# Performance work log

Hardware: AMD Instinct MI355X
Metric: run time of the kernel (lower is better)

Reference implementation:

```python
import jax, jax.numpy as jnp
import numpy as np

DIM = 1024
DEPTH = 6
HEADS = 16
DH = 64
INNER = HEADS * DH  # 1024
MLP = 4096
B, N = 2, 2048
SCALE = DH ** (-0.5)  # 0.125; module divides softmax output by this (x8)
EPS = 1e-5


def setup_inputs() -> dict:
    key = jax.random.key(0)
    ks = jax.random.split(key, 5)
    s = jnp.float32(0.02)
    return {
        "x": jax.random.normal(ks[0], (B, N, DIM), dtype=jnp.float32),
        "ln1_g": jnp.ones((DEPTH, DIM), jnp.float32),
        "ln1_b": jnp.zeros((DEPTH, DIM), jnp.float32),
        "w_qkv": jax.random.normal(ks[1], (DEPTH, DIM, 3 * INNER), jnp.float32) * s,
        "w_out": jax.random.normal(ks[2], (DEPTH, INNER, DIM), jnp.float32) * s,
        "b_out": jnp.zeros((DEPTH, DIM), jnp.float32),
        "ln2_g": jnp.ones((DEPTH, DIM), jnp.float32),
        "ln2_b": jnp.zeros((DEPTH, DIM), jnp.float32),
        "w1": jax.random.normal(ks[3], (DEPTH, DIM, MLP), jnp.float32) * s,
        "b1": jnp.zeros((DEPTH, MLP), jnp.float32),
        "w2": jax.random.normal(ks[4], (DEPTH, MLP, DIM), jnp.float32) * s,
        "b2": jnp.zeros((DEPTH, DIM), jnp.float32),
    }


def _layernorm(x, g, b):
    m = x.mean(-1, keepdims=True)
    v = ((x - m) ** 2).mean(-1, keepdims=True)
    return (x - m) * jax.lax.rsqrt(v + EPS) * g + b


def _attention(x, w_qkv, w_out, b_out):
    b, n, _ = x.shape
    qkv = x @ w_qkv  # [b, n, 3*inner]
    q, k, v = jnp.split(qkv, 3, axis=-1)

    def heads(t):
        return t.reshape(b, n, HEADS, DH).transpose(0, 2, 1, 3)  # [b,h,n,d]

    q, k, v = heads(q), heads(k), heads(v)
    # Faithful to source: softmax of UNSCALED logits, then divide by scale.
    score = jax.nn.softmax(jnp.einsum("bhqd,bhkd->bhqk", q, k), axis=-1) / SCALE
    o = jnp.einsum("bhqk,bhkd->bhqd", score, v)
    o = o.transpose(0, 2, 1, 3).reshape(b, n, INNER)
    return o @ w_out + b_out


def reference(x, ln1_g, ln1_b, w_qkv, w_out, b_out, ln2_g, ln2_b, w1, b1, w2, b2):
    def layer(h, p):
        g1, bb1, wq, wo, bo, g2, bb2, ww1, bw1, ww2, bw2 = p
        h = h + _attention(_layernorm(h, g1, bb1), wq, wo, bo)
        f = _layernorm(h, g2, bb2) @ ww1 + bw1
        f = jax.nn.gelu(f, approximate=False)  # nn.GELU default = exact erf
        h = h + f @ ww2 + bw2
        return h, None

    out, _ = jax.lax.scan(
        layer, x, (ln1_g, ln1_b, w_qkv, w_out, b_out, ln2_g, ln2_b, w1, b1, w2, b2)
    )
    return out
```

## Files before the change

kernel.cpp:

```cpp
#include <hip/hip_runtime.h>
#include <cstdint>

typedef __attribute__((ext_vector_type(4))) float f32x4;
typedef __attribute__((ext_vector_type(8))) short short8;
typedef __attribute__((ext_vector_type(4))) short short4v;
typedef _Float16 half8v __attribute__((ext_vector_type(8)));

__device__ __forceinline__ unsigned short f2h(float x) {
  _Float16 h = (_Float16)x;
  return __builtin_bit_cast(unsigned short, h);
}
__device__ __forceinline__ unsigned int pk2(float a, float b) {
  auto h = __builtin_amdgcn_cvt_pkrtz(a, b);
  return __builtin_bit_cast(unsigned int, h);
}

template <typename V>
__device__ __forceinline__ auto mfma_impl(V a, V b, f32x4 c, int)
    -> decltype(__builtin_amdgcn_mfma_f32_16x16x32_f16(a, b, c, 0, 0, 0)) {
  return __builtin_amdgcn_mfma_f32_16x16x32_f16(a, b, c, 0, 0, 0);
}
template <typename V>
__device__ __forceinline__ f32x4 mfma_impl(V a, V b, f32x4 c, long) {
  return __builtin_amdgcn_mfma_f32_16x16x32_f16(
      __builtin_bit_cast(half8v, a), __builtin_bit_cast(half8v, b), c, 0, 0, 0);
}
__device__ __forceinline__ f32x4 MFMA(short8 a, short8 b, f32x4 c) {
  return mfma_impl(a, b, c, 0);
}

__device__ __forceinline__ void load_lds16(const void* g, void* l) {
  __builtin_amdgcn_global_load_lds(
      (__attribute__((address_space(1))) void*)(uintptr_t)g,
      (__attribute__((address_space(3))) void*)l, 16, 0, 0);
}

__global__ __launch_bounds__(256) void ln_f16_kernel(
    const float* __restrict__ X, const float* __restrict__ gam,
    const float* __restrict__ bet, unsigned short* __restrict__ Y) {
  __shared__ float red[8];
  const int row = blockIdx.x, t = threadIdx.x;
  const float4 v = ((const float4*)(X + (size_t)row * 1024))[t];
  float s = v.x + v.y + v.z + v.w;
#pragma unroll
  for (int o = 32; o >= 1; o >>= 1) s += __shfl_xor(s, o, 64);
  if ((t & 63) == 0) red[t >> 6] = s;
  __syncthreads();
  const float mean = (red[0] + red[1] + red[2] + red[3]) * (1.0f / 1024.0f);
  const float dx = v.x - mean, dy = v.y - mean, dz = v.z - mean, dw = v.w - mean;
  float ss = dx * dx + dy * dy + dz * dz + dw * dw;
#pragma unroll
  for (int o = 32; o >= 1; o >>= 1) ss += __shfl_xor(ss, o, 64);
  if ((t & 63) == 0) red[4 + (t >> 6)] = ss;
  __syncthreads();
  const float var = (red[4] + red[5] + red[6] + red[7]) * (1.0f / 1024.0f);
  const float rstd = rsqrtf(var + 1e-5f);
  const float4 gg = ((const float4*)gam)[t];
  const float4 bb = ((const float4*)bet)[t];
  ushort4 o4;
  o4.x = f2h(dx * rstd * gg.x + bb.x);
  o4.y = f2h(dy * rstd * gg.y + bb.y);
  o4.z = f2h(dz * rstd * gg.z + bb.z);
  o4.w = f2h(dw * rstd * gg.w + bb.w);
  ((ushort4*)(Y + (size_t)row * 1024))[t] = o4;
}

__global__ __launch_bounds__(256) void transpose_f16_kernel(
    const float* __restrict__ W, unsigned short* __restrict__ WT, int K, int N) {
  __shared__ float t[32][33];
  const int n0 = blockIdx.x * 32, k0 = blockIdx.y * 32;
  const int tx = threadIdx.x, ty = threadIdx.y;
#pragma unroll
  for (int i = 0; i < 4; ++i)
    t[ty + 8 * i][tx] = W[(size_t)(k0 + ty + 8 * i) * N + n0 + tx];
  __syncthreads();
#pragma unroll
  for (int i = 0; i < 4; ++i)
    WT[(size_t)(n0 + ty + 8 * i) * K + k0 + tx] = f2h(t[tx][ty + 8 * i]);
}

__global__ __launch_bounds__(256) void vt_transpose_kernel(
    const unsigned short* __restrict__ qkvb, unsigned short* __restrict__ VT) {
  __shared__ unsigned short t[32][33];
  const int c0 = blockIdx.x * 32;
  const int r0 = blockIdx.y * 32;
  const int b = blockIdx.z;
  const int tx = threadIdx.x, ty = threadIdx.y;
  const size_t base = (size_t)b * 2048;
#pragma unroll
  for (int i = 0; i < 4; ++i)
    t[ty + 8 * i][tx] = qkvb[(base + r0 + ty + 8 * i) * 3072 + 2048 + c0 + tx];
  __syncthreads();
#pragma unroll
  for (int i = 0; i < 4; ++i)
    VT[((size_t)b * 1024 + c0 + ty + 8 * i) * 2048 + r0 + tx] = t[tx][ty + 8 * i];
}

template <int BM, int EPI>
__global__ __launch_bounds__(256, BM == 64 ? 3 : 2) void gemm_f16_kernel(
    const unsigned short* __restrict__ A, const unsigned short* __restrict__ BT,
    void* Cout, const float* __restrict__ bias, const float* __restrict__ res,
    int M, int N, int K) {
  constexpr int BN = 128, BK = 64;
  constexpr int MR = BM / 32;
  constexpr int ACH = BM * BK / 8;
  constexpr int BCH = BN * BK / 8;
  __shared__ alignas(16) unsigned short a_sh[2][BM * BK];
  __shared__ alignas(16) unsigned short b_sh[2][BN * BK];
  const int tid = threadIdx.x;
  const int w = tid >> 6, lane = tid & 63, g = lane >> 4, lm = lane & 15;
  const int m0 = blockIdx.y * BM, n0 = blockIdx.x * BN;
  const int wm = (w >> 1) * (BM / 2), wn = (w & 1) * 64;
  f32x4 acc[MR][4] = {};
  const int nsteps = K >> 6;

  auto stage = [&](int buf, int kk) {
#pragma unroll
    for (int c0 = 0; c0 < ACH; c0 += 256) {
      const int c = c0 + tid, row = c >> 3;
      const int sc = (c & 7) ^ (row & 7);
      const int cb = c0 + (tid & 192);
      load_lds16(A + (size_t)(m0 + row) * K + kk + sc * 8, &a_sh[buf][cb * 8]);
    }
#pragma unroll
    for (int c0 = 0; c0 < BCH; c0 += 256) {
      const int c = c0 + tid, row = c >> 3;
      const int sc = (c & 7) ^ (row & 7);
      const int cb = c0 + (tid & 192);
      load_lds16(BT + (size_t)(n0 + row) * K + kk + sc * 8, &b_sh[buf][cb * 8]);
    }
  };

  stage(0, 0);
  __syncthreads();
  int cur = 0;
  for (int step = 0; step < nsteps; ++step) {
    if (step + 1 < nsteps) stage(cur ^ 1, (step + 1) * BK);
#pragma unroll
    for (int kc = 0; kc < 2; ++kc) {
      short8 af[MR], bfr[4];
#pragma unroll
      for (int i = 0; i < MR; ++i) {
        const int r = wm + i * 16 + lm;
        af[i] = *(const short8*)&a_sh[cur][r * 64 + (((kc << 2) | g) ^ (r & 7)) * 8];
      }
#pragma unroll
      for (int j = 0; j < 4; ++j) {
        const int r = wn + j * 16 + lm;
        bfr[j] = *(const short8*)&b_sh[cur][r * 64 + (((kc << 2) | g) ^ (r & 7)) * 8];
      }
#pragma unroll
      for (int i = 0; i < MR; ++i)
#pragma unroll
        for (int j = 0; j < 4; ++j)
          acc[i][j] = MFMA(af[i], bfr[j], acc[i][j]);
    }
    if (step + 1 < nsteps) {
      __syncthreads();
      cur ^= 1;
    }
  }

#pragma unroll
  for (int i = 0; i < MR; ++i) {
    const int row = m0 + wm + i * 16 + g * 4;
#pragma unroll
    for (int j = 0; j < 4; ++j) {
      const int col = n0 + wn + j * 16 + lm;
#pragma unroll
      for (int r = 0; r < 4; ++r) {
        const float v = acc[i][j][r];
        const size_t idx = (size_t)(row + r) * N + col;
        if (EPI == 0) {
          ((unsigned short*)Cout)[idx] = f2h(v);
        } else if (EPI == 1) {
          const float xx = v + bias[col];
          ((unsigned short*)Cout)[idx] =
              f2h(0.5f * xx * (1.0f + erff(xx * 0.70710678118654752f)));
        } else {
          ((float*)Cout)[idx] = res[idx] + v + bias[col];
        }
      }
    }
  }
}

__global__ __launch_bounds__(256) void attn_kernel(
    const unsigned short* __restrict__ qkv, const unsigned short* __restrict__ vt,
    unsigned short* __restrict__ obuf) {
  constexpr int PK = 72;
  constexpr int PV = 68;
  __shared__ alignas(16) unsigned short Qs[64 * PK];
  __shared__ alignas(16) unsigned short Ks[64 * PK];
  __shared__ alignas(16) unsigned short VsT[64 * PV];
  const int tid = threadIdx.x;
  const int w = tid >> 6, lane = tid & 63, g = lane >> 4, lm = lane & 15;
  const int qbase = blockIdx.x * 64, h = blockIdx.y, b = blockIdx.z;
  const size_t rowbase = (size_t)b * 2048;
  const int r0 = tid >> 3, cc = tid & 7;
  const int vd = tid >> 2, vk = tid & 3;
  const int kdst = r0 * PK + cc * 8;

  const unsigned short* qptr = qkv + (rowbase + qbase + r0) * 3072 + h * 64 + cc * 8;
#pragma unroll
  for (int s = 0; s < 2; ++s)
    *(uint4*)&Qs[(s * 32 + r0) * PK + cc * 8] = *(const uint4*)(qptr + (size_t)s * 32 * 3072);

  const unsigned short* kptr = qkv + (rowbase + r0) * 3072 + 1024 + h * 64 + cc * 8;
  const unsigned short* vtp = vt + ((size_t)b * 1024 + h * 64 + vd) * 2048 + vk * 16;
  uint4 kreg[2], vreg[2];
  auto load_tile = [&](int n) {
#pragma unroll
    for (int s = 0; s < 2; ++s) {
      kreg[s] = *(const uint4*)(kptr + (size_t)n * 64 * 3072 + (size_t)s * 32 * 3072);
      vreg[s] = *(const uint4*)(vtp + n * 64 + s * 8);
    }
  };
  auto write_tile = [&]() {
#pragma unroll
    for (int s = 0; s < 2; ++s) {
      *(uint4*)&Ks[kdst + s * 32 * PK] = kreg[s];
      uint2 lo; lo.x = vreg[s].x; lo.y = vreg[s].y;
      uint2 hi; hi.x = vreg[s].z; hi.y = vreg[s].w;
      *(uint2*)&VsT[vd * PV + vk * 16 + s * 8] = lo;
      *(uint2*)&VsT[vd * PV + vk * 16 + s * 8 + 4] = hi;
    }
  };

  load_tile(0);
  __syncthreads();
  short8 qf[2];
#pragma unroll
  for (int s2 = 0; s2 < 2; ++s2)
    qf[s2] = *(const short8*)&Qs[(w * 16 + lm) * PK + s2 * 32 + g * 8];

  float mrun = -1e30f, lrun = 0.0f;
  f32x4 accO[4] = {};

  for (int n = 0; n < 32; ++n) {
    __syncthreads();
    write_tile();
    __syncthreads();
    if (n + 1 < 32) load_tile(n + 1);

    f32x4 sf[4] = {};
    __builtin_amdgcn_s_setprio(1);
#pragma unroll
    for (int s2 = 0; s2 < 2; ++s2)
#pragma unroll
      for (int i = 0; i < 4; ++i) {
        const short8 kf = *(const short8*)&Ks[(i * 16 + lm) * PK + s2 * 32 + g * 8];
        sf[i] = MFMA(kf, qf[s2], sf[i]);
      }
    __builtin_amdgcn_s_setprio(0);

    float tmax = -1e30f;
#pragma unroll
    for (int i = 0; i < 4; ++i)
#pragma unroll
      for (int r = 0; r < 4; ++r) tmax = fmaxf(tmax, sf[i][r]);
    tmax = fmaxf(tmax, __shfl_xor(tmax, 16, 64));
    tmax = fmaxf(tmax, __shfl_xor(tmax, 32, 64));
    const float mnew = fmaxf(mrun, tmax);
    const float scale = __expf(mrun - mnew);
    float p[4][4];
    float psum = 0.0f;
#pragma unroll
    for (int i = 0; i < 4; ++i)
#pragma unroll
      for (int r = 0; r < 4; ++r) {
        p[i][r] = __expf(sf[i][r] - mnew);
        psum += p[i][r];
      }
    psum += __shfl_xor(psum, 16, 64);
    psum += __shfl_xor(psum, 32, 64);
    lrun = lrun * scale + psum;
    mrun = mnew;
#pragma unroll
    for (int t = 0; t < 4; ++t) accO[t] = accO[t] * scale;

    uint4 pbu[2];
#pragma unroll
    for (int blk = 0; blk < 2; ++blk) {
      pbu[blk].x = pk2(p[2 * blk][0], p[2 * blk][1]);
      pbu[blk].y = pk2(p[2 * blk][2], p[2 * blk][3]);
      pbu[blk].z = pk2(p[2 * blk + 1][0], p[2 * blk + 1][1]);
      pbu[blk].w = pk2(p[2 * blk + 1][2], p[2 * blk + 1][3]);
    }

    __builtin_amdgcn_s_setprio(1);
#pragma unroll
    for (int blk = 0; blk < 2; ++blk) {
      const short8 pbv = __builtin_bit_cast(short8, pbu[blk]);
#pragma unroll
      for (int t = 0; t < 4; ++t) {
        const int base = (16 * t + lm) * PV + 32 * blk + 4 * g;
        const short4v vlo = *(const short4v*)&VsT[base];
        const short4v vhi = *(const short4v*)&VsT[base + 16];
        const short8 vf = {vlo[0], vlo[1], vlo[2], vlo[3],
                           vhi[0], vhi[1], vhi[2], vhi[3]};
        accO[t] = MFMA(vf, pbv, accO[t]);
      }
    }
    __builtin_amdgcn_s_setprio(0);
  }

  const float inv = 8.0f / lrun;
  const size_t orow = rowbase + qbase + w * 16 + lm;
#pragma unroll
  for (int t = 0; t < 4; ++t) {
    ushort4 o4;
    o4.x = f2h(accO[t][0] * inv);
    o4.y = f2h(accO[t][1] * inv);
    o4.z = f2h(accO[t][2] * inv);
    o4.w = f2h(accO[t][3] * inv);
    *(ushort4*)&obuf[orow * 1024 + h * 64 + t * 16 + g * 4] = o4;
  }
}

extern "C" void kernel_launch(void* const* d_in, const int* in_sizes, int n_in,
                              void* d_out, int out_size, void* d_ws, size_t ws_size,
                              hipStream_t stream) {
  const float* x     = (const float*)d_in[0];
  const float* ln1_g = (const float*)d_in[1];
  const float* ln1_b = (const float*)d_in[2];
  const float* w_qkv = (const float*)d_in[3];
  const float* w_out = (const float*)d_in[4];
  const float* b_out = (const float*)d_in[5];
  const float* ln2_g = (const float*)d_in[6];
  const float* ln2_b = (const float*)d_in[7];
  const float* w1    = (const float*)d_in[8];
  const float* b1    = (const float*)d_in[9];
  const float* w2    = (const float*)d_in[10];
  const float* b2    = (const float*)d_in[11];
  float* h = (float*)d_out;

  char* ws = (char*)d_ws;
  const size_t MB = 1u << 20;
  unsigned short* xn   = (unsigned short*)(ws);
  unsigned short* ob   = (unsigned short*)(ws + 8 * MB);
  unsigned short* qkvb = (unsigned short*)(ws + 16 * MB);
  unsigned short* mid  = (unsigned short*)(ws + 40 * MB);
  unsigned short* wt   = (unsigned short*)(ws + 72 * MB);

  hipError_t e0 = hipMemcpyAsync(h, x, (size_t)4096 * 1024 * sizeof(float),
                                 hipMemcpyDeviceToDevice, stream);
  (void)e0;

  const dim3 tb(32, 8);
  for (int L = 0; L < 6; ++L) {
    const float* Lg1 = ln1_g + L * 1024;
    const float* Lb1 = ln1_b + L * 1024;
    const float* Lwq = w_qkv + (size_t)L * 1024 * 3072;
    const float* Lwo = w_out + (size_t)L * 1024 * 1024;
    const float* Lbo = b_out + L * 1024;
    const float* Lg2 = ln2_g + L * 1024;
    const float* Lb2 = ln2_b + L * 1024;
    const float* Lw1 = w1 + (size_t)L * 1024 * 4096;
    const float* Lb1m = b1 + L * 4096;
    const float* Lw2 = w2 + (size_t)L * 4096 * 1024;
    const float* Lb2m = b2 + L * 1024;

    ln_f16_kernel<<<4096, 256, 0, stream>>>(h, Lg1, Lb1, xn);
    transpose_f16_kernel<<<dim3(96, 32), tb, 0, stream>>>(Lwq, wt, 1024, 3072);
    gemm_f16_kernel<128, 0><<<dim3(24, 32), 256, 0, stream>>>(
        xn, wt, qkvb, nullptr, nullptr, 4096, 3072, 1024);
    vt_transpose_kernel<<<dim3(32, 64, 2), tb, 0, stream>>>(qkvb, xn);
    attn_kernel<<<dim3(32, 16, 2), 256, 0, stream>>>(qkvb, xn, ob);
    transpose_f16_kernel<<<dim3(32, 32), tb, 0, stream>>>(Lwo, wt, 1024, 1024);
    gemm_f16_kernel<64, 2><<<dim3(8, 64), 256, 0, stream>>>(
        ob, wt, h, Lbo, h, 4096, 1024, 1024);

    ln_f16_kernel<<<4096, 256, 0, stream>>>(h, Lg2, Lb2, xn);
    transpose_f16_kernel<<<dim3(128, 32), tb, 0, stream>>>(Lw1, wt, 1024, 4096);
    gemm_f16_kernel<128, 1><<<dim3(32, 32), 256, 0, stream>>>(
        xn, wt, mid, Lb1m, nullptr, 4096, 4096, 1024);
    transpose_f16_kernel<<<dim3(32, 128), tb, 0, stream>>>(Lw2, wt, 4096, 1024);
    gemm_f16_kernel<64, 2><<<dim3(8, 64), 256, 0, stream>>>(
        mid, wt, h, Lb2m, h, 4096, 1024, 4096);
  }
  (void)in_sizes; (void)n_in; (void)out_size; (void)ws_size;
}
```

Baseline: 1.845 ms.

## Merge per-layer weight transposes into one launch and widen attention KV tile

The four per-layer weight transpose/convert launches are merged into a single kernel that dispatches on block index and writes into separate workspace regions. This removes three launches per layer. The attention kernel now processes 128 keys per iteration instead of 64, halving the loop trips and barriers. It drops the separate Q shared buffer by staging Q in the K buffer, and loads V with wider 16-byte vectors. The larger tile raises register pressure, and the kernel now carries a launch-bounds occupancy hint of 4.

```diff
diff --git a/kernel.cpp b/kernel.cpp
--- a/kernel.cpp
+++ b/kernel.cpp
@@ -65,18 +65,28 @@
   ((ushort4*)(Y + (size_t)row * 1024))[t] = o4;
 }
 
-__global__ __launch_bounds__(256) void transpose_f16_kernel(
-    const float* __restrict__ W, unsigned short* __restrict__ WT, int K, int N) {
+__global__ __launch_bounds__(256) void transpose_all_kernel(
+    const float* __restrict__ wq, const float* __restrict__ wo,
+    const float* __restrict__ w1, const float* __restrict__ w2,
+    unsigned short* __restrict__ wtq, unsigned short* __restrict__ wto,
+    unsigned short* __restrict__ wt1, unsigned short* __restrict__ wt2) {
   __shared__ float t[32][33];
-  const int n0 = blockIdx.x * 32, k0 = blockIdx.y * 32;
+  int i = blockIdx.x;
+  const float* W; unsigned short* WT; int K, N;
+  if (i < 3072)      { W = wq; WT = wtq; K = 1024; N = 3072; }
+  else if (i < 4096) { i -= 3072; W = wo; WT = wto; K = 1024; N = 1024; }
+  else if (i < 8192) { i -= 4096; W = w1; WT = wt1; K = 1024; N = 4096; }
+  else               { i -= 8192; W = w2; WT = wt2; K = 4096; N = 1024; }
+  const int nt = N >> 5;
+  const int n0 = (i % nt) * 32, k0 = (i / nt) * 32;
   const int tx = threadIdx.x, ty = threadIdx.y;
 #pragma unroll
-  for (int i = 0; i < 4; ++i)
-    t[ty + 8 * i][tx] = W[(size_t)(k0 + ty + 8 * i) * N + n0 + tx];
-  __syncthreads();
-#pragma unroll
-  for (int i = 0; i < 4; ++i)
-    WT[(size_t)(n0 + ty + 8 * i) * K + k0 + tx] = f2h(t[tx][ty + 8 * i]);
+  for (int j = 0; j < 4; ++j)
+    t[ty + 8 * j][tx] = W[(size_t)(k0 + ty + 8 * j) * N + n0 + tx];
+  __syncthreads();
+#pragma unroll
+  for (int j = 0; j < 4; ++j)
+    WT[(size_t)(n0 + ty + 8 * j) * K + k0 + tx] = f2h(t[tx][ty + 8 * j]);
 }
 
 __global__ __launch_bounds__(256) void vt_transpose_kernel(
@@ -185,46 +195,44 @@
   }
 }
 
-__global__ __launch_bounds__(256) void attn_kernel(
+__global__ __launch_bounds__(256, 4) void attn_kernel(
     const unsigned short* __restrict__ qkv, const unsigned short* __restrict__ vt,
     unsigned short* __restrict__ obuf) {
   constexpr int PK = 72;
-  constexpr int PV = 68;
-  __shared__ alignas(16) unsigned short Qs[64 * PK];
-  __shared__ alignas(16) unsigned short Ks[64 * PK];
-  __shared__ alignas(16) unsigned short VsT[64 * PV];
+  constexpr int PV2 = 136;
+  __shared__ alignas(16) unsigned short Ks[128 * PK];
+  __shared__ alignas(16) unsigned short VsT[64 * PV2];
   const int tid = threadIdx.x;
   const int w = tid >> 6, lane = tid & 63, g = lane >> 4, lm = lane & 15;
   const int qbase = blockIdx.x * 64, h = blockIdx.y, b = blockIdx.z;
   const size_t rowbase = (size_t)b * 2048;
   const int r0 = tid >> 3, cc = tid & 7;
-  const int vd = tid >> 2, vk = tid & 3;
+  const int vd = tid >> 4, ch = tid & 15;
   const int kdst = r0 * PK + cc * 8;
 
   const unsigned short* qptr = qkv + (rowbase + qbase + r0) * 3072 + h * 64 + cc * 8;
 #pragma unroll
   for (int s = 0; s < 2; ++s)
-    *(uint4*)&Qs[(s * 32 + r0) * PK + cc * 8] = *(const uint4*)(qptr + (size_t)s * 32 * 3072);
+    *(uint4*)&Ks[(s * 32 + r0) * PK + cc * 8] = *(const uint4*)(qptr + (size_t)s * 32 * 3072);
 
   const unsigned short* kptr = qkv + (rowbase + r0) * 3072 + 1024 + h * 64 + cc * 8;
-  const unsigned short* vtp = vt + ((size_t)b * 1024 + h * 64 + vd) * 2048 + vk * 16;
-  uint4 kreg[2], vreg[2];
+  const unsigned short* vtp = vt + ((size_t)b * 1024 + h * 64 + vd) * 2048 + ch * 8;
+  uint4 kreg[4], vreg[4];
   auto load_tile = [&](int n) {
 #pragma unroll
-    for (int s = 0; s < 2; ++s) {
-      kreg[s] = *(const uint4*)(kptr + (size_t)n * 64 * 3072 + (size_t)s * 32 * 3072);
-      vreg[s] = *(const uint4*)(vtp + n * 64 + s * 8);
-    }
+    for (int s = 0; s < 4; ++s)
+      kreg[s] = *(const uint4*)(kptr + ((size_t)n * 128 + s * 32) * 3072);
+#pragma unroll
+    for (int s = 0; s < 4; ++s)
+      vreg[s] = *(const uint4*)(vtp + (size_t)s * 16 * 2048 + n * 128);
   };
   auto write_tile = [&]() {
 #pragma unroll
-    for (int s = 0; s < 2; ++s) {
-      *(uint4*)&Ks[kdst + s * 32 * PK] = kreg[s];
-      uint2 lo; lo.x = vreg[s].x; lo.y = vreg[s].y;
-      uint2 hi; hi.x = vreg[s].z; hi.y = vreg[s].w;
-      *(uint2*)&VsT[vd * PV + vk * 16 + s * 8] = lo;
-      *(uint2*)&VsT[vd * PV + vk * 16 + s * 8 + 4] = hi;
-    }
+    for (int s = 0; s < 4; ++s)
+      *(uint4*)&Ks[(s * 32 + r0) * PK + cc * 8] = kreg[s];
+#pragma unroll
+    for (int s = 0; s < 4; ++s)
+      *(uint4*)&VsT[(s * 16 + vd) * PV2 + ch * 8] = vreg[s];
   };
 
   load_tile(0);
@@ -232,23 +240,23 @@
   short8 qf[2];
 #pragma unroll
   for (int s2 = 0; s2 < 2; ++s2)
-    qf[s2] = *(const short8*)&Qs[(w * 16 + lm) * PK + s2 * 32 + g * 8];
+    qf[s2] = *(const short8*)&Ks[(w * 16 + lm) * PK + s2 * 32 + g * 8];
 
   float mrun = -1e30f, lrun = 0.0f;
   f32x4 accO[4] = {};
 
-  for (int n = 0; n < 32; ++n) {
+  for (int n = 0; n < 16; ++n) {
     __syncthreads();
     write_tile();
     __syncthreads();
-    if (n + 1 < 32) load_tile(n + 1);
-
-    f32x4 sf[4] = {};
+    if (n + 1 < 16) load_tile(n + 1);
+
+    f32x4 sf[8] = {};
     __builtin_amdgcn_s_setprio(1);
 #pragma unroll
     for (int s2 = 0; s2 < 2; ++s2)
 #pragma unroll
-      for (int i = 0; i < 4; ++i) {
+      for (int i = 0; i < 8; ++i) {
         const short8 kf = *(const short8*)&Ks[(i * 16 + lm) * PK + s2 * 32 + g * 8];
         sf[i] = MFMA(kf, qf[s2], sf[i]);
       }
@@ -256,22 +264,33 @@
 
     float tmax = -1e30f;
 #pragma unroll
-    for (int i = 0; i < 4; ++i)
+    for (int i = 0; i < 8; ++i)
 #pragma unroll
       for (int r = 0; r < 4; ++r) tmax = fmaxf(tmax, sf[i][r]);
     tmax = fmaxf(tmax, __shfl_xor(tmax, 16, 64));
     tmax = fmaxf(tmax, __shfl_xor(tmax, 32, 64));
     const float mnew = fmaxf(mrun, tmax);
     const float scale = __expf(mrun - mnew);
-    float p[4][4];
     float psum = 0.0f;
-#pragma unroll
-    for (int i = 0; i < 4; ++i)
+    uint4 pbu[4];
+#pragma unroll
+    for (int blk = 0; blk < 4; ++blk) {
+      float p0[4], p1[4];
 #pragma unroll
       for (int r = 0; r < 4; ++r) {
-        p[i][r] = __expf(sf[i][r] - mnew);
-        psum += p[i][r];
-      }
+        p0[r] = __expf(sf[2 * blk][r] - mnew);
+        psum += p0[r];
+      }
+#pragma unroll
+      for (int r = 0; r < 4; ++r) {
+        p1[r] = __expf(sf[2 * blk + 1][r] - mnew);
+        psum += p1[r];
+      }
+      pbu[blk].x = pk2(p0[0], p0[1]);
+      pbu[blk].y = pk2(p0[2], p0[3]);
+      pbu[blk].z = pk2(p1[0], p1[1]);
+      pbu[blk].w = pk2(p1[2], p1[3]);
+    }
     psum += __shfl_xor(psum, 16, 64);
     psum += __shfl_xor(psum, 32, 64);
     lrun = lrun * scale + psum;
@@ -279,22 +298,13 @@
 #pragma unroll
     for (int t = 0; t < 4; ++t) accO[t] = accO[t] * scale;
 
-    uint4 pbu[2];
-#pragma unroll
-    for (int blk = 0; blk < 2; ++blk) {
-      pbu[blk].x = pk2(p[2 * blk][0], p[2 * blk][1]);
-      pbu[blk].y = pk2(p[2 * blk][2], p[2 * blk][3]);
-      pbu[blk].z = pk2(p[2 * blk + 1][0], p[2 * blk + 1][1]);
-      pbu[blk].w = pk2(p[2 * blk + 1][2], p[2 * blk + 1][3]);
-    }
-
     __builtin_amdgcn_s_setprio(1);
 #pragma unroll
-    for (int blk = 0; blk < 2; ++blk) {
+    for (int blk = 0; blk < 4; ++blk) {
       const short8 pbv = __builtin_bit_cast(short8, pbu[blk]);
 #pragma unroll
       for (int t = 0; t < 4; ++t) {
-        const int base = (16 * t + lm) * PV + 32 * blk + 4 * g;
+        const int base = (16 * t + lm) * PV2 + 32 * blk + 4 * g;
         const short4v vlo = *(const short4v*)&VsT[base];
         const short4v vhi = *(const short4v*)&VsT[base + 16];
         const short8 vf = {vlo[0], vlo[1], vlo[2], vlo[3],
@@ -342,6 +352,10 @@
   unsigned short* qkvb = (unsigned short*)(ws + 16 * MB);
   unsigned short* mid  = (unsigned short*)(ws + 40 * MB);
   unsigned short* wt   = (unsigned short*)(ws + 72 * MB);
+  unsigned short* wtq = wt;
+  unsigned short* wto = wt + 3145728;
+  unsigned short* wt1 = wt + 4194304;
+  unsigned short* wt2 = wt + 8388608;
 
   hipError_t e0 = hipMemcpyAsync(h, x, (size_t)4096 * 1024 * sizeof(float),
                                  hipMemcpyDeviceToDevice, stream);
@@ -361,23 +375,22 @@
     const float* Lw2 = w2 + (size_t)L * 4096 * 1024;
     const float* Lb2m = b2 + L * 1024;
 
+    transpose_all_kernel<<<12288, tb, 0, stream>>>(
+        Lwq, Lwo, Lw1, Lw2, wtq, wto, wt1, wt2);
+
     ln_f16_kernel<<<4096, 256, 0, stream>>>(h, Lg1, Lb1, xn);
-    transpose_f16_kernel<<<dim3(96, 32), tb, 0, stream>>>(Lwq, wt, 1024, 3072);
     gemm_f16_kernel<128, 0><<<dim3(24, 32), 256, 0, stream>>>(
-        xn, wt, qkvb, nullptr, nullptr, 4096, 3072, 1024);
+        xn, wtq, qkvb, nullptr, nullptr, 4096, 3072, 1024);
     vt_transpose_kernel<<<dim3(32, 64, 2), tb, 0, stream>>>(qkvb, xn);
     attn_kernel<<<dim3(32, 16, 2), 256, 0, stream>>>(qkvb, xn, ob);
-    transpose_f16_kernel<<<dim3(32, 32), tb, 0, stream>>>(Lwo, wt, 1024, 1024);
     gemm_f16_kernel<64, 2><<<dim3(8, 64), 256, 0, stream>>>(
-        ob, wt, h, Lbo, h, 4096, 1024, 1024);
+        ob, wto, h, Lbo, h, 4096, 1024, 1024);
 
     ln_f16_kernel<<<4096, 256, 0, stream>>>(h, Lg2, Lb2, xn);
-    transpose_f16_kernel<<<dim3(128, 32), tb, 0, stream>>>(Lw1, wt, 1024, 4096);
     gemm_f16_kernel<128, 1><<<dim3(32, 32), 256, 0, stream>>>(
-        xn, wt, mid, Lb1m, nullptr, 4096, 4096, 1024);
-    transpose_f16_kernel<<<dim3(32, 128), tb, 0, stream>>>(Lw2, wt, 4096, 1024);
+        xn, wt1, mid, Lb1m, nullptr, 4096, 4096, 1024);
     gemm_f16_kernel<64, 2><<<dim3(8, 64), 256, 0, stream>>>(
-        mid, wt, h, Lb2m, h, 4096, 1024, 4096);
+        mid, wt2, h, Lb2m, h, 4096, 1024, 4096);
   }
   (void)in_sizes; (void)n_in; (void)out_size; (void)ws_size;
 }
```

Result: slower. 2.208 ms (+19.7%).

## Split attention over two key chunks and batch weight transposes per layer

Applied to the files above, without the earlier changes.

Attention now splits the key sequence into two halves, launching twice as many blocks. Each block writes unnormalized partial outputs plus running max and sum, and a new combine kernel merges them with a log-sum-exp rescale. Separately, the four per-layer weight transposes are merged into one launch that writes into separate buffers. This cuts launch count, though the combine pass adds extra global memory traffic and fp16 partial outputs risk a small loss of precision.

```diff
diff --git a/kernel.cpp b/kernel.cpp
--- a/kernel.cpp
+++ b/kernel.cpp
@@ -9,6 +9,9 @@
 __device__ __forceinline__ unsigned short f2h(float x) {
   _Float16 h = (_Float16)x;
   return __builtin_bit_cast(unsigned short, h);
+}
+__device__ __forceinline__ float h2f(unsigned short u) {
+  return (float)__builtin_bit_cast(_Float16, u);
 }
 __device__ __forceinline__ unsigned int pk2(float a, float b) {
   auto h = __builtin_amdgcn_cvt_pkrtz(a, b);
@@ -65,18 +68,28 @@
   ((ushort4*)(Y + (size_t)row * 1024))[t] = o4;
 }
 
-__global__ __launch_bounds__(256) void transpose_f16_kernel(
-    const float* __restrict__ W, unsigned short* __restrict__ WT, int K, int N) {
+__global__ __launch_bounds__(256) void transpose_all_kernel(
+    const float* __restrict__ wq, const float* __restrict__ wo,
+    const float* __restrict__ w1, const float* __restrict__ w2,
+    unsigned short* __restrict__ wtq, unsigned short* __restrict__ wto,
+    unsigned short* __restrict__ wt1, unsigned short* __restrict__ wt2) {
   __shared__ float t[32][33];
-  const int n0 = blockIdx.x * 32, k0 = blockIdx.y * 32;
+  int i = blockIdx.x;
+  const float* W; unsigned short* WT; int K, N;
+  if (i < 3072)      { W = wq; WT = wtq; K = 1024; N = 3072; }
+  else if (i < 4096) { i -= 3072; W = wo; WT = wto; K = 1024; N = 1024; }
+  else if (i < 8192) { i -= 4096; W = w1; WT = wt1; K = 1024; N = 4096; }
+  else               { i -= 8192; W = w2; WT = wt2; K = 4096; N = 1024; }
+  const int nt = N >> 5;
+  const int n0 = (i % nt) * 32, k0 = (i / nt) * 32;
   const int tx = threadIdx.x, ty = threadIdx.y;
 #pragma unroll
-  for (int i = 0; i < 4; ++i)
-    t[ty + 8 * i][tx] = W[(size_t)(k0 + ty + 8 * i) * N + n0 + tx];
-  __syncthreads();
-#pragma unroll
-  for (int i = 0; i < 4; ++i)
-    WT[(size_t)(n0 + ty + 8 * i) * K + k0 + tx] = f2h(t[tx][ty + 8 * i]);
+  for (int j = 0; j < 4; ++j)
+    t[ty + 8 * j][tx] = W[(size_t)(k0 + ty + 8 * j) * N + n0 + tx];
+  __syncthreads();
+#pragma unroll
+  for (int j = 0; j < 4; ++j)
+    WT[(size_t)(n0 + ty + 8 * j) * K + k0 + tx] = f2h(t[tx][ty + 8 * j]);
 }
 
 __global__ __launch_bounds__(256) void vt_transpose_kernel(
@@ -187,7 +200,7 @@
 
 __global__ __launch_bounds__(256) void attn_kernel(
     const unsigned short* __restrict__ qkv, const unsigned short* __restrict__ vt,
-    unsigned short* __restrict__ obuf) {
+    unsigned short* __restrict__ opart, float2* __restrict__ stats) {
   constexpr int PK = 72;
   constexpr int PV = 68;
   __shared__ alignas(16) unsigned short Qs[64 * PK];
@@ -195,7 +208,8 @@
   __shared__ alignas(16) unsigned short VsT[64 * PV];
   const int tid = threadIdx.x;
   const int w = tid >> 6, lane = tid & 63, g = lane >> 4, lm = lane & 15;
-  const int qbase = blockIdx.x * 64, h = blockIdx.y, b = blockIdx.z;
+  const int qbase = blockIdx.x * 64, h = blockIdx.y;
+  const int b = blockIdx.z & 1, chunk = blockIdx.z >> 1;
   const size_t rowbase = (size_t)b * 2048;
   const int r0 = tid >> 3, cc = tid & 7;
   const int vd = tid >> 2, vk = tid & 3;
@@ -206,8 +220,10 @@
   for (int s = 0; s < 2; ++s)
     *(uint4*)&Qs[(s * 32 + r0) * PK + cc * 8] = *(const uint4*)(qptr + (size_t)s * 32 * 3072);
 
-  const unsigned short* kptr = qkv + (rowbase + r0) * 3072 + 1024 + h * 64 + cc * 8;
-  const unsigned short* vtp = vt + ((size_t)b * 1024 + h * 64 + vd) * 2048 + vk * 16;
+  const unsigned short* kptr =
+      qkv + (rowbase + chunk * 1024 + r0) * 3072 + 1024 + h * 64 + cc * 8;
+  const unsigned short* vtp =
+      vt + ((size_t)b * 1024 + h * 64 + vd) * 2048 + chunk * 1024 + vk * 16;
   uint4 kreg[2], vreg[2];
   auto load_tile = [&](int n) {
 #pragma unroll
@@ -237,11 +253,11 @@
   float mrun = -1e30f, lrun = 0.0f;
   f32x4 accO[4] = {};
 
-  for (int n = 0; n < 32; ++n) {
+  for (int n = 0; n < 16; ++n) {
     __syncthreads();
     write_tile();
     __syncthreads();
-    if (n + 1 < 32) load_tile(n + 1);
+    if (n + 1 < 16) load_tile(n + 1);
 
     f32x4 sf[4] = {};
     __builtin_amdgcn_s_setprio(1);
@@ -305,17 +321,41 @@
     __builtin_amdgcn_s_setprio(0);
   }
 
-  const float inv = 8.0f / lrun;
-  const size_t orow = rowbase + qbase + w * 16 + lm;
+  const int qrow = qbase + w * 16 + lm;
+  const size_t orow = rowbase + qrow;
 #pragma unroll
   for (int t = 0; t < 4; ++t) {
     ushort4 o4;
-    o4.x = f2h(accO[t][0] * inv);
-    o4.y = f2h(accO[t][1] * inv);
-    o4.z = f2h(accO[t][2] * inv);
-    o4.w = f2h(accO[t][3] * inv);
-    *(ushort4*)&obuf[orow * 1024 + h * 64 + t * 16 + g * 4] = o4;
+    o4.x = f2h(accO[t][0]);
+    o4.y = f2h(accO[t][1]);
+    o4.z = f2h(accO[t][2]);
+    o4.w = f2h(accO[t][3]);
+    *(ushort4*)&opart[(size_t)chunk * 4194304 + orow * 1024 + h * 64 + t * 16 + g * 4] = o4;
   }
+  if (g == 0)
+    stats[((size_t)(chunk * 2 + b) * 16 + h) * 2048 + qrow] = make_float2(mrun, lrun);
+}
+
+__global__ __launch_bounds__(256) void attn_combine_kernel(
+    const unsigned short* __restrict__ op, const float2* __restrict__ stats,
+    unsigned short* __restrict__ ob) {
+  const int row = blockIdx.x;
+  const int col0 = threadIdx.x * 4;
+  const int b = row >> 11, qrow = row & 2047, h = col0 >> 6;
+  const float2 s0 = stats[((size_t)b * 16 + h) * 2048 + qrow];
+  const float2 s1 = stats[((size_t)(2 + b) * 16 + h) * 2048 + qrow];
+  const float m = fmaxf(s0.x, s1.x);
+  const float w0 = __expf(s0.x - m), w1 = __expf(s1.x - m);
+  const float sc = 8.0f / (s0.y * w0 + s1.y * w1);
+  const size_t i = (size_t)row * 1024 + col0;
+  const ushort4 a0 = *(const ushort4*)&op[i];
+  const ushort4 a1 = *(const ushort4*)&op[4194304 + i];
+  ushort4 o;
+  o.x = f2h((h2f(a0.x) * w0 + h2f(a1.x) * w1) * sc);
+  o.y = f2h((h2f(a0.y) * w0 + h2f(a1.y) * w1) * sc);
+  o.z = f2h((h2f(a0.z) * w0 + h2f(a1.z) * w1) * sc);
+  o.w = f2h((h2f(a0.w) * w0 + h2f(a1.w) * w1) * sc);
+  *(ushort4*)&ob[i] = o;
 }
 
 extern "C" void kernel_launch(void* const* d_in, const int* in_sizes, int n_in,
@@ -342,6 +382,11 @@
   unsigned short* qkvb = (unsigned short*)(ws + 16 * MB);
   unsigned short* mid  = (unsigned short*)(ws + 40 * MB);
   unsigned short* wt   = (unsigned short*)(ws + 72 * MB);
+  float2* stats = (float2*)(ws + 56 * MB);
+  unsigned short* wtq = wt;
+  unsigned short* wto = wt + 3145728;
+  unsigned short* wt1 = wt + 4194304;
+  unsigned short* wt2 = wt + 8388608;
 
   hipError_t e0 = hipMemcpyAsync(h, x, (size_t)4096 * 1024 * sizeof(float),
                                  hipMemcpyDeviceToDevice, stream);
@@ -361,23 +406,23 @@
     const float* Lw2 = w2 + (size_t)L * 4096 * 1024;
     const float* Lb2m = b2 + L * 1024;
 
+    transpose_all_kernel<<<12288, tb, 0, stream>>>(
+        Lwq, Lwo, Lw1, Lw2, wtq, wto, wt1, wt2);
+
     ln_f16_kernel<<<4096, 256, 0, stream>>>(h, Lg1, Lb1, xn);
-    transpose_f16_kernel<<<dim3(96, 32), tb, 0, stream>>>(Lwq, wt, 1024, 3072);
     gemm_f16_kernel<128, 0><<<dim3(24, 32), 256, 0, stream>>>(
-        xn, wt, qkvb, nullptr, nullptr, 4096, 3072, 1024);
+        xn, wtq, qkvb, nullptr, nullptr, 4096, 3072, 1024);
     vt_transpose_kernel<<<dim3(32, 64, 2), tb, 0, stream>>>(qkvb, xn);
-    attn_kernel<<<dim3(32, 16, 2), 256, 0, stream>>>(qkvb, xn, ob);
-    transpose_f16_kernel<<<dim3(32, 32), tb, 0, stream>>>(Lwo, wt, 1024, 1024);
+    attn_kernel<<<dim3(32, 16, 4), 256, 0, stream>>>(qkvb, xn, mid, stats);
+    attn_combine_kernel<<<4096, 256, 0, stream>>>(mid, stats, ob);
     gemm_f16_kernel<64, 2><<<dim3(8, 64), 256, 0, stream>>>(
-        ob, wt, h, Lbo, h, 4096, 1024, 1024);
+        ob, wto, h, Lbo, h, 4096, 1024, 1024);
 
     ln_f16_kernel<<<4096, 256, 0, stream>>>(h, Lg2, Lb2, xn);
-    transpose_f16_kernel<<<dim3(128, 32), tb, 0, stream>>>(Lw1, wt, 1024, 4096);
     gemm_f16_kernel<128, 1><<<dim3(32, 32), 256, 0, stream>>>(
-        xn, wt, mid, Lb1m, nullptr, 4096, 4096, 1024);
-    transpose_f16_kernel<<<dim3(32, 128), tb, 0, stream>>>(Lw2, wt, 4096, 1024);
+        xn, wt1, mid, Lb1m, nullptr, 4096, 4096, 1024);
     gemm_f16_kernel<64, 2><<<dim3(8, 64), 256, 0, stream>>>(
-        mid, wt, h, Lb2m, h, 4096, 1024, 4096);
+        mid, wt2, h, Lb2m, h, 4096, 1024, 4096);
   }
   (void)in_sizes; (void)n_in; (void)out_size; (void)ws_size;
 }
```

After: 1.857 ms. About the same (+0.7%).
